# Kernel tuning notes

Hardware: AMD Instinct MI355X
Metric: run time of the kernel (lower is better)

The kernel has to match this reference:

```python
import jax, jax.numpy as jnp
import numpy as np

RAD_ORDER = 15
ANG_ORDER = 7
RAD_CUTOFF = 6.0
ANG_CUTOFF = 4.0
MIN_CUTOFF = 0.55
N_SPECIES = 2
N_ATOMS = 10000
MAX_NB = 32


def _typespin(n_species):
    # matches Fortran: even n skips zero -> {-1, 1} for 2 species
    vals = []
    s = int(-n_species / 2)
    for _ in range(n_species):
        if s == 0 and n_species % 2 == 0:
            s += 1
        vals.append(float(s))
        s += 1
    return jnp.asarray(vals, dtype=jnp.float32)


def _cheby_stack(x, order):
    # T_0..T_order of x, stacked on last axis
    Ts = [jnp.ones_like(x), x]
    for _ in range(2, order + 1):
        Ts.append(2.0 * x * Ts[-1] - Ts[-2])
    return jnp.stack(Ts[: order + 1], axis=-1)


def setup_inputs() -> dict:
    key = jax.random.key(0)
    k1, k2, k3 = jax.random.split(key, 3)
    positions = jax.random.normal(k1, (N_ATOMS, 3), dtype=jnp.float32) * 5.0
    species_indices = jax.random.randint(k2, (N_ATOMS,), 0, N_SPECIES)
    neighbor_indices = jax.random.randint(k3, (N_ATOMS, MAX_NB), 0, N_ATOMS)
    neighbor_vectors = jax.random.normal(jax.random.fold_in(key, 7), (N_ATOMS, MAX_NB, 3), dtype=jnp.float32) * 2.5
    return {
        "positions": positions,
        "species_indices": species_indices,
        "neighbor_indices": neighbor_indices,
        "neighbor_vectors": neighbor_vectors,
    }


def _features(positions, species_indices, neighbor_indices, neighbor_vectors):
    typespin = _typespin(N_SPECIES)
    ts_nb = typespin[species_indices[neighbor_indices]]  # [N, M]

    d = jnp.linalg.norm(neighbor_vectors, axis=-1)  # [N, M]
    d_safe = jnp.maximum(d, 1e-8)

    # ---------- radial ----------
    mask_r = ((d <= RAD_CUTOFF) & (d > MIN_CUTOFF)).astype(d.dtype)  # [N, M]
    x_r = jnp.clip(2.0 * (d - MIN_CUTOFF) / (RAD_CUTOFF - MIN_CUTOFF) - 1.0, -1.0, 1.0)
    fc_r = 0.5 * (jnp.cos(jnp.pi * jnp.minimum(d, RAD_CUTOFF) / RAD_CUTOFF) + 1.0)
    G_rad = _cheby_stack(x_r, RAD_ORDER) * (fc_r * mask_r)[..., None]  # [N, M, n_rad]
    rad_unw = G_rad.sum(axis=1)                          # [N, n_rad]
    rad_w = (G_rad * ts_nb[..., None]).sum(axis=1)       # [N, n_rad]

    # ---------- angular ----------
    mask_a = ((d <= ANG_CUTOFF) & (d > MIN_CUTOFF)).astype(d.dtype)  # [N, M]
    fc_a = 0.5 * (jnp.cos(jnp.pi * jnp.minimum(d, ANG_CUTOFF) / ANG_CUTOFF) + 1.0) * mask_a
    unit = neighbor_vectors / d_safe[..., None]          # [N, M, 3]
    cos = jnp.clip(jnp.einsum("nmd,nkd->nmk", unit, unit), -1.0, 1.0)  # [N, M, M]
    triu = jnp.triu(jnp.ones((MAX_NB, MAX_NB), dtype=d.dtype), k=1)
    w = fc_a[:, :, None] * fc_a[:, None, :] * triu       # [N, M, M] pair weight, j<k only
    w_ts = w * ts_nb[:, :, None] * ts_nb[:, None, :]

    # Chebyshev recurrence over cos(theta); accumulate per order to avoid [N,M,M,n_ang]
    ang_unw, ang_w = [], []
    T_prev = jnp.ones_like(cos)
    T_cur = cos
    for n in range(ANG_ORDER + 1):
        T_n = T_prev if n == 0 else (T_cur if n == 1 else 2.0 * cos * T_cur - T_prev)
        if n >= 2:
            T_prev, T_cur = T_cur, T_n
        ang_unw.append(jnp.einsum("nmk,nmk->n", w, T_n))
        ang_w.append(jnp.einsum("nmk,nmk->n", w_ts, T_n))
    ang_unw = jnp.stack(ang_unw, axis=1)  # [N, n_ang]
    ang_w = jnp.stack(ang_w, axis=1)

    # feature layout: [rad_unweighted, rad_typespin, ang_unweighted, ang_typespin]
    return jnp.concatenate([rad_unw, rad_w, ang_unw, ang_w], axis=1)  # [N, 48]


def reference(positions, species_indices, neighbor_indices, neighbor_vectors):
    return _features(positions, species_indices, neighbor_indices, neighbor_vectors)
```

## Files before the change

kernel.cpp:

```cpp
#include <hip/hip_runtime.h>

#define NATOMS 10000
#define MAXNB  32
#define NRAD   16
#define NANG   8
#define WPB    4
#define RSTR   36

#define WAVE_LDS_FENCE() asm volatile("s_waitcnt lgkmcnt(0)" ::: "memory")

__global__ __launch_bounds__(256, 6) void cheby_desc_kernel(
    const int*   __restrict__ species,
    const int*   __restrict__ nb_idx,
    const float* __restrict__ nb_vec,
    float*       __restrict__ out)
{
    const int lane = threadIdx.x & 63;
    const int wv   = threadIdx.x >> 6;
    const int sub  = lane >> 5;
    const int nb   = lane & 31;
    const int abase = blockIdx.x * (WPB * 2) + wv * 2;
    const int atom  = abase + sub;

    __shared__ float4 nbd4[WPB][64];
    __shared__ float  tsb[WPB][64];
    __shared__ float  red[WPB][32][RSTR];

    const float* vp = nb_vec + (size_t)(atom * MAXNB + nb) * 3;
    const float vx = vp[0], vy = vp[1], vz = vp[2];
    const int   ni = nb_idx[atom * MAXNB + nb];
    const float ts = (float)(2 * species[ni] - 1);

    const float d     = __builtin_amdgcn_sqrtf(vx * vx + vy * vy + vz * vz);
    const float inv_d = __builtin_amdgcn_rcpf(fmaxf(d, 1e-8f));
    const float ux = vx * inv_d, uy = vy * inv_d, uz = vz * inv_d;
    const float PI = 3.14159265358979323846f;

    const float fca = ((d <= 4.0f) && (d > 0.55f))
                    ? 0.5f * (__cosf(fminf(d, 4.0f) * (PI / 4.0f)) + 1.0f) : 0.0f;
    const float fcats = fca * ts;

    nbd4[wv][lane] = make_float4(ux, uy, uz, fcats);
    tsb[wv][lane]  = ts;

    {
        float xr = 2.0f * (d - 0.55f) * (1.0f / 5.45f) - 1.0f;
        xr = fminf(fmaxf(xr, -1.0f), 1.0f);
        const float fcr = 0.5f * (__cosf(fminf(d, 6.0f) * (PI / 6.0f)) + 1.0f);
        const float g = ((d <= 6.0f) && (d > 0.55f)) ? fcr : 0.0f;
        float* rb = &red[wv][sub * 16][nb];
        rb[0]    = g;
        rb[RSTR] = g * xr;
        float Tp = 1.0f, Tc = xr;
        const float x2 = xr + xr;
        #pragma unroll
        for (int n = 2; n < NRAD; ++n) {
            const float Tn = x2 * Tc - Tp;
            rb[n * RSTR] = g * Tn;
            Tp = Tc; Tc = Tn;
        }
    }
    WAVE_LDS_FENCE();

    {
        const int j = lane >> 1, h = lane & 1;
        const int s = j >> 4,  c = j & 15;
        const float* rr = &red[wv][j][h * 16];
        const float* tr = &tsb[wv][s * 32 + h * 16];
        float sU = 0.0f, sW = 0.0f;
        #pragma unroll
        for (int i = 0; i < 4; ++i) {
            const float4 r4 = *(const float4*)(rr + 4 * i);
            const float4 t4 = *(const float4*)(tr + 4 * i);
            sU += (r4.x + r4.y) + (r4.z + r4.w);
            sW += t4.x * r4.x + t4.y * r4.y + t4.z * r4.z + t4.w * r4.w;
        }
        sU += __shfl_xor(sU, 1, 64);
        sW += __shfl_xor(sW, 1, 64);
        if (h == 0) {
            out[(abase + s) * 48 + c]      = sU;
            out[(abase + s) * 48 + 16 + c] = sW;
        }
    }

    float aU[NANG], aW[NANG];
    #pragma unroll
    for (int n = 0; n < NANG; ++n) { aU[n] = 0.0f; aW[n] = 0.0f; }

    const int kb = sub * 32;
    #pragma unroll
    for (int o = 1; o <= 16; ++o) {
        const int k = kb + ((nb + o) & 31);
        const float4 K = nbd4[wv][k];
        float c = ux * K.x + uy * K.y + uz * K.z;
        c = fminf(fmaxf(c, -1.0f), 1.0f);
        float wts = fcats * K.w;
        float w   = fabsf(wts);
        if (o == 16) { w *= 0.5f; wts *= 0.5f; }
        const float c2 = c + c;
        float Ta = 1.0f, Tb = c;
        aU[0] += w;     aW[0] += wts;
        aU[1] += w * c; aW[1] += wts * c;
        #pragma unroll
        for (int n = 2; n < NANG; ++n) {
            const float Tn = c2 * Tb - Ta;
            aU[n] += w * Tn;  aW[n] += wts * Tn;
            Ta = Tb; Tb = Tn;
        }
    }

    WAVE_LDS_FENCE();
    {
        float* ab = &red[wv][sub * 16][nb];
        #pragma unroll
        for (int n = 0; n < NANG; ++n) {
            ab[n * RSTR]       = aU[n];
            ab[(8 + n) * RSTR] = aW[n];
        }
    }
    WAVE_LDS_FENCE();

    {
        const int j = lane >> 1, h = lane & 1;
        const int s = j >> 4,  jj = j & 15;
        const float* rr = &red[wv][j][h * 16];
        float sv = 0.0f;
        #pragma unroll
        for (int i = 0; i < 4; ++i) {
            const float4 r4 = *(const float4*)(rr + 4 * i);
            sv += (r4.x + r4.y) + (r4.z + r4.w);
        }
        sv += __shfl_xor(sv, 1, 64);
        if (h == 0) out[(abase + s) * 48 + 32 + jj] = sv;
    }
}

extern "C" void kernel_launch(void* const* d_in, const int* in_sizes, int n_in,
                              void* d_out, int out_size, void* d_ws, size_t ws_size,
                              hipStream_t stream) {
    const int*   species = (const int*)  d_in[1];
    const int*   nbidx   = (const int*)  d_in[2];
    const float* nbvec   = (const float*)d_in[3];
    float*       out     = (float*)      d_out;

    const int blocks = NATOMS / (WPB * 2);
    cheby_desc_kernel<<<blocks, 256, 0, stream>>>(species, nbidx, nbvec, out);
}
```

Baseline: 11.09 us.

## Map one atom per wavefront, splitting radial weighting and angular pairs across half-waves

Each wavefront now handles a single atom instead of two. The lower half-wave writes unweighted radial terms and the upper half writes typespin-weighted ones into one shared reduction row, which removes the separate typespin buffer and the multiply in the reduction. The angular pair loop is split so each half-wave covers 8 of the 16 offsets, halving per-lane angular work. The cost is twice as many blocks, redundant vector and species loads in the upper half-wave, and twice the total lane count.

New measurement: 12.24 us. 1.1x slower.

```diff
diff --git a/kernel.cpp b/kernel.cpp
--- a/kernel.cpp
+++ b/kernel.cpp
@@ -5,7 +5,7 @@
 #define NRAD   16
 #define NANG   8
 #define WPB    4
-#define RSTR   36
+#define ROWW   68
 
 #define WAVE_LDS_FENCE() asm volatile("s_waitcnt lgkmcnt(0)" ::: "memory")
 
@@ -17,19 +17,17 @@
 {
     const int lane = threadIdx.x & 63;
     const int wv   = threadIdx.x >> 6;
-    const int sub  = lane >> 5;
     const int nb   = lane & 31;
-    const int abase = blockIdx.x * (WPB * 2) + wv * 2;
-    const int atom  = abase + sub;
+    const int hi   = lane >> 5;
+    const int atom = blockIdx.x * WPB + wv;
 
-    __shared__ float4 nbd4[WPB][64];
-    __shared__ float  tsb[WPB][64];
-    __shared__ float  red[WPB][32][RSTR];
+    __shared__ float4 nbd4[WPB][MAXNB];
+    __shared__ float  red[WPB][16][ROWW];
 
     const float* vp = nb_vec + (size_t)(atom * MAXNB + nb) * 3;
     const float vx = vp[0], vy = vp[1], vz = vp[2];
     const int   ni = nb_idx[atom * MAXNB + nb];
-    const float ts = (float)(2 * species[ni] - 1);
+    const float ts = species[ni] ? 1.0f : -1.0f;
 
     const float d     = __builtin_amdgcn_sqrtf(vx * vx + vy * vy + vz * vz);
     const float inv_d = __builtin_amdgcn_rcpf(fmaxf(d, 1e-8f));
@@ -40,57 +38,48 @@
                     ? 0.5f * (__cosf(fminf(d, 4.0f) * (PI / 4.0f)) + 1.0f) : 0.0f;
     const float fcats = fca * ts;
 
-    nbd4[wv][lane] = make_float4(ux, uy, uz, fcats);
-    tsb[wv][lane]  = ts;
+    if (hi == 0) nbd4[wv][nb] = make_float4(ux, uy, uz, fcats);
 
     {
         float xr = 2.0f * (d - 0.55f) * (1.0f / 5.45f) - 1.0f;
         xr = fminf(fmaxf(xr, -1.0f), 1.0f);
         const float fcr = 0.5f * (__cosf(fminf(d, 6.0f) * (PI / 6.0f)) + 1.0f);
-        const float g = ((d <= 6.0f) && (d > 0.55f)) ? fcr : 0.0f;
-        float* rb = &red[wv][sub * 16][nb];
+        float g = ((d <= 6.0f) && (d > 0.55f)) ? fcr : 0.0f;
+        if (hi) g *= ts;
+        float* rb = &red[wv][0][lane];
         rb[0]    = g;
-        rb[RSTR] = g * xr;
+        rb[ROWW] = g * xr;
         float Tp = 1.0f, Tc = xr;
         const float x2 = xr + xr;
         #pragma unroll
         for (int n = 2; n < NRAD; ++n) {
             const float Tn = x2 * Tc - Tp;
-            rb[n * RSTR] = g * Tn;
+            rb[n * ROWW] = g * Tn;
             Tp = Tc; Tc = Tn;
         }
     }
     WAVE_LDS_FENCE();
 
     {
-        const int j = lane >> 1, h = lane & 1;
-        const int s = j >> 4,  c = j & 15;
-        const float* rr = &red[wv][j][h * 16];
-        const float* tr = &tsb[wv][s * 32 + h * 16];
-        float sU = 0.0f, sW = 0.0f;
-        #pragma unroll
-        for (int i = 0; i < 4; ++i) {
-            const float4 r4 = *(const float4*)(rr + 4 * i);
-            const float4 t4 = *(const float4*)(tr + 4 * i);
-            sU += (r4.x + r4.y) + (r4.z + r4.w);
-            sW += t4.x * r4.x + t4.y * r4.y + t4.z * r4.z + t4.w * r4.w;
-        }
-        sU += __shfl_xor(sU, 1, 64);
-        sW += __shfl_xor(sW, 1, 64);
-        if (h == 0) {
-            out[(abase + s) * 48 + c]      = sU;
-            out[(abase + s) * 48 + 16 + c] = sW;
-        }
+        const int t = lane >> 1, h = lane & 1;
+        const int c = t & 15, g2 = t >> 4;
+        const float4* rr = (const float4*)&red[wv][c][g2 * 32 + h * 16];
+        const float4 r0 = rr[0], r1 = rr[1], r2 = rr[2], r3 = rr[3];
+        float sv = (((r0.x + r0.y) + (r0.z + r0.w)) + ((r1.x + r1.y) + (r1.z + r1.w)))
+                 + (((r2.x + r2.y) + (r2.z + r2.w)) + ((r3.x + r3.y) + (r3.z + r3.w)));
+        sv += __shfl_xor(sv, 1, 64);
+        if (h == 0) out[atom * 48 + g2 * 16 + c] = sv;
     }
 
     float aU[NANG], aW[NANG];
     #pragma unroll
     for (int n = 0; n < NANG; ++n) { aU[n] = 0.0f; aW[n] = 0.0f; }
 
-    const int kb = sub * 32;
+    const int obase = 1 + 8 * hi;
     #pragma unroll
-    for (int o = 1; o <= 16; ++o) {
-        const int k = kb + ((nb + o) & 31);
+    for (int i = 0; i < 8; ++i) {
+        const int o = obase + i;
+        const int k = (nb + o) & 31;
         const float4 K = nbd4[wv][k];
         float c = ux * K.x + uy * K.y + uz * K.z;
         c = fminf(fmaxf(c, -1.0f), 1.0f);
@@ -111,27 +100,24 @@
 
     WAVE_LDS_FENCE();
     {
-        float* ab = &red[wv][sub * 16][nb];
+        float* ab = &red[wv][0][lane];
         #pragma unroll
         for (int n = 0; n < NANG; ++n) {
-            ab[n * RSTR]       = aU[n];
-            ab[(8 + n) * RSTR] = aW[n];
+            ab[n * ROWW]       = aU[n];
+            ab[(8 + n) * ROWW] = aW[n];
         }
     }
     WAVE_LDS_FENCE();
 
     {
-        const int j = lane >> 1, h = lane & 1;
-        const int s = j >> 4,  jj = j & 15;
-        const float* rr = &red[wv][j][h * 16];
-        float sv = 0.0f;
-        #pragma unroll
-        for (int i = 0; i < 4; ++i) {
-            const float4 r4 = *(const float4*)(rr + 4 * i);
-            sv += (r4.x + r4.y) + (r4.z + r4.w);
-        }
+        const int f = lane >> 2, h = lane & 3;
+        const float4* rr = (const float4*)&red[wv][f][h * 16];
+        const float4 r0 = rr[0], r1 = rr[1], r2 = rr[2], r3 = rr[3];
+        float sv = (((r0.x + r0.y) + (r0.z + r0.w)) + ((r1.x + r1.y) + (r1.z + r1.w)))
+                 + (((r2.x + r2.y) + (r2.z + r2.w)) + ((r3.x + r3.y) + (r3.z + r3.w)));
         sv += __shfl_xor(sv, 1, 64);
-        if (h == 0) out[(abase + s) * 48 + 32 + jj] = sv;
+        sv += __shfl_xor(sv, 2, 64);
+        if (h == 0) out[atom * 48 + 32 + f] = sv;
     }
 }
 
@@ -143,6 +129,6 @@
     const float* nbvec   = (const float*)d_in[3];
     float*       out     = (float*)      d_out;
 
-    const int blocks = NATOMS / (WPB * 2);
+    const int blocks = NATOMS / WPB;
     cheby_desc_kernel<<<blocks, 256, 0, stream>>>(species, nbidx, nbvec, out);
 }
```
